# Optimization experiments

Hardware: AMD Instinct MI355X
Metric: run time of the kernel (lower is better)

## Reference

```python
import jax, jax.numpy as jnp
import numpy as np

N_HEADS = 16
HEAD_DIM = 128
ROPE_DIM = 64
ROPE_BASE = 10000.0


def _rope(x, base):
    # x: (B, H, S, dim) -- standard rotate-half RoPE, positions = arange(S)
    B, H, S, dim = x.shape
    inv_freq = 1.0 / (base ** (jnp.arange(0, dim, 2, dtype=jnp.float32) / dim))
    pos = jnp.arange(S, dtype=jnp.float32)
    freqs = pos[:, None] * inv_freq[None, :]                  # (S, dim/2)
    emb = jnp.concatenate([freqs, freqs], axis=-1)            # (S, dim)
    cos = jnp.cos(emb).astype(x.dtype)[None, None]
    sin = jnp.sin(emb).astype(x.dtype)[None, None]
    x1, x2 = x[..., : dim // 2], x[..., dim // 2 :]
    rot = jnp.concatenate([-x2, x1], axis=-1)
    return x * cos + rot * sin


def setup_inputs() -> dict:
    key = jax.random.key(0)
    ks = jax.random.split(key, 7)
    B, S, D = 2, 2048, 2048
    s = 0.02
    return {
        "x": jax.random.normal(ks[0], (B, S, D), jnp.float32),
        "Wq": jax.random.normal(ks[1], (D, N_HEADS * HEAD_DIM), jnp.float32) * s,
        "Wq_rope": jax.random.normal(ks[2], (D, N_HEADS * ROPE_DIM), jnp.float32) * s,
        "Wkv_down": jax.random.normal(ks[3], (D, 512), jnp.float32) * s,
        "Wkv_up": jax.random.normal(ks[4], (512, 2 * N_HEADS * HEAD_DIM), jnp.float32) * s,
        "Wk_rope": jax.random.normal(ks[5], (D, ROPE_DIM), jnp.float32) * s,
        "Wo": jax.random.normal(ks[6], (D, D), jnp.float32) * s,
    }


def reference(x, Wq, Wq_rope, Wkv_down, Wkv_up, Wk_rope, Wo):
    B, S, D = x.shape
    H, hd, rd = N_HEADS, HEAD_DIM, ROPE_DIM

    # content and decoupled-RoPE queries
    q_c = (x @ Wq).reshape(B, S, H, hd).transpose(0, 2, 1, 3)        # (B,H,S,hd)
    q_r = (x @ Wq_rope).reshape(B, S, H, rd).transpose(0, 2, 1, 3)   # (B,H,S,rd)
    q_r = _rope(q_r, ROPE_BASE)

    # low-rank KV latent + shared rope key
    c_kv = x @ Wkv_down                                              # (B,S,r)
    k_r = _rope((x @ Wk_rope)[:, None, :, :], ROPE_BASE)             # (B,1,S,rd)

    kv = c_kv @ Wkv_up                                               # (B,S,2*H*hd)
    k_c, v = jnp.split(kv, 2, axis=-1)
    k_c = k_c.reshape(B, S, H, hd).transpose(0, 2, 1, 3)             # (B,H,S,hd)
    v = v.reshape(B, S, H, hd).transpose(0, 2, 1, 3)                 # (B,H,S,hd)

    q_full = jnp.concatenate([q_c, q_r], axis=-1)                    # (B,H,S,hd+rd)
    k_full = jnp.concatenate([k_c, jnp.broadcast_to(k_r, (B, H, S, rd))], axis=-1)

    scale = 1.0 / np.sqrt(hd + rd).astype(np.float32)
    scores = jnp.einsum("bhqd,bhkd->bhqk", q_full, k_full) * scale   # (B,H,S,S)
    mask = jnp.tril(jnp.ones((S, S), dtype=bool))
    scores = jnp.where(mask[None, None], scores, jnp.finfo(scores.dtype).min)
    attn = jax.nn.softmax(scores, axis=-1)

    out = jnp.einsum("bhqk,bhkd->bhqd", attn, v)                     # (B,H,S,hd)
    out = out.transpose(0, 2, 1, 3).reshape(B, S, D)
    return out @ Wo
```

## Files before the change

### kernel.cpp

```cpp
#include <hip/hip_runtime.h>
#include <hip/hip_bf16.h>
#include <cstdint>
#include <cstddef>

typedef unsigned short u16;
typedef __attribute__((ext_vector_type(8))) short short8;
typedef __attribute__((ext_vector_type(4))) float f32x4;
typedef __attribute__((ext_vector_type(16))) float f32x16;

__device__ __forceinline__ u16 f2bf(float f) {
    union { float f; uint32_t u; } v; v.f = f;
    uint32_t u = v.u;
    return (u16)((u + 0x7fffu + ((u >> 16) & 1u)) >> 16);
}
__device__ __forceinline__ float bf2f(u16 u) {
    union { uint32_t u; float f; } v; v.u = ((uint32_t)u) << 16;
    return v.f;
}
__device__ __forceinline__ float exp2_hw(float x) {
    float r;
    asm("v_exp_f32 %0, %1" : "=v"(r) : "v"(x));
    return r;
}
__device__ __forceinline__ uint32_t cvtpk(float lo, float hi) {
    uint32_t r;
    asm("v_cvt_pk_bf16_f32 %0, %1, %2" : "=v"(r) : "v"(lo), "v"(hi));
    return r;
}
__device__ __forceinline__ void permswap(uint32_t& a, uint32_t& b) {
    asm("v_permlane32_swap_b32 %0, %1" : "+v"(a), "+v"(b));
}
__device__ __forceinline__ float xhalf_max(float x) {
    union { float f; uint32_t u; } a, b; a.f = x; b.f = x;
    permswap(a.u, b.u);
    return fmaxf(a.f, b.f);
}
__device__ __forceinline__ float xhalf_sum(float x) {
    union { float f; uint32_t u; } a, b; a.f = x; b.f = x;
    permswap(a.u, b.u);
    return a.f + b.f;
}

__device__ __forceinline__ void async_cp16(const u16* g, u16* l) {
    __builtin_amdgcn_global_load_lds(
        (const __attribute__((address_space(1))) unsigned int*)g,
        (__attribute__((address_space(3))) unsigned int*)l, 16, 0, 0);
}

__global__ __launch_bounds__(256) void cast_f32_bf16(const float* __restrict__ in,
                                                     u16* __restrict__ out, int n) {
    int i = (blockIdx.x * 256 + threadIdx.x) * 4;
    if (i >= n) return;
    float4 v = *(const float4*)(in + i);
    ushort4 r;
    r.x = f2bf(v.x); r.y = f2bf(v.y); r.z = f2bf(v.z); r.w = f2bf(v.w);
    *(ushort4*)(out + i) = r;
}

__global__ __launch_bounds__(256) void transpose_cast(const float* __restrict__ W,
                                                      u16* __restrict__ Wt, int K, int N,
                                                      float smul) {
    __shared__ u16 tile[64][72];
    int kt = blockIdx.x * 64, nt = blockIdx.y * 64;
    int t = threadIdx.x;
#pragma unroll
    for (int i = 0; i < 16; i++) {
        int idx = t + i * 256; int kl = idx >> 6, nl = idx & 63;
        tile[kl][nl] = f2bf(W[(size_t)(kt + kl) * N + nt + nl] * smul);
    }
    __syncthreads();
#pragma unroll
    for (int i = 0; i < 16; i++) {
        int idx = t + i * 256; int nl = idx >> 6, kl = idx & 63;
        Wt[(size_t)(nt + nl) * K + kt + kl] = tile[kl][nl];
    }
}

template <int OUTF32, int KDIM, int NDIM>
__global__ __launch_bounds__(256) void gemm_bt(const u16* __restrict__ A, int lda,
                                               const u16* __restrict__ Bt,
                                               void* __restrict__ Cout, int ldc) {
    __shared__ __align__(16) u16 Al[128 * 32];
    __shared__ __align__(16) u16 Bl[128 * 32];
    int m0 = blockIdx.x * 128, n0 = blockIdx.y * 128;
    int t = threadIdx.x;
    int w = t >> 6, l = t & 63;
    int lm = l & 15, lq = l >> 4;
    int wm = (w >> 1) * 64, wn = (w & 1) * 64;
    f32x4 acc[4][4] = {};

    for (int k0 = 0; k0 < KDIM; k0 += 32) {
#pragma unroll
        for (int c = 0; c < 2; c++) {
            int chunk = w * 128 + c * 64 + l;
            int row = chunk >> 2, col8 = (chunk & 3) * 8;
            async_cp16(A + (size_t)(m0 + row) * lda + k0 + col8,
                       Al + (w * 128 + c * 64) * 8);
            int brow = n0 + row;
            if (NDIM % 128 != 0) { if (brow >= NDIM) brow = NDIM - 1; }
            async_cp16(Bt + (size_t)brow * KDIM + k0 + col8,
                       Bl + (w * 128 + c * 64) * 8);
        }
        __syncthreads();
        short8 af[4], bfr[4];
#pragma unroll
        for (int mt = 0; mt < 4; mt++)
            af[mt] = *(const short8*)(Al + (wm + mt * 16 + lm) * 32 + lq * 8);
#pragma unroll
        for (int nt = 0; nt < 4; nt++)
            bfr[nt] = *(const short8*)(Bl + (wn + nt * 16 + lm) * 32 + lq * 8);
#pragma unroll
        for (int mt = 0; mt < 4; mt++)
#pragma unroll
            for (int nt = 0; nt < 4; nt++)
                acc[mt][nt] = __builtin_amdgcn_mfma_f32_16x16x32_bf16(af[mt], bfr[nt], acc[mt][nt], 0, 0, 0);
        __syncthreads();
    }
#pragma unroll
    for (int mt = 0; mt < 4; mt++) {
#pragma unroll
        for (int nt = 0; nt < 4; nt++) {
            int col = n0 + wn + nt * 16 + lm;
            if (col < NDIM) {
#pragma unroll
                for (int r = 0; r < 4; r++) {
                    int row = m0 + wm + mt * 16 + lq * 4 + r;
                    if (OUTF32) ((float*)Cout)[(size_t)row * ldc + col] = acc[mt][nt][r];
                    else        ((u16*)Cout)[(size_t)row * ldc + col] = f2bf(acc[mt][nt][r]);
                }
            }
        }
    }
}

template <int KDIM>
__global__ __launch_bounds__(256, 2) void gemm_rg(const u16* __restrict__ A, int lda,
                                                  const u16* __restrict__ Bt,
                                                  u16* __restrict__ C, int ldc) {
    __shared__ __align__(16) u16 Ab[3][128 * 32];
    __shared__ __align__(16) u16 Bb[3][256 * 32];
    const int nk = KDIM / 32;
    int m0 = blockIdx.x * 128, n0 = blockIdx.y * 256;
    int t = threadIdx.x, w = t >> 6, l = t & 63;
    int lm = l & 15, lq = l >> 4;
    int wn = w * 64;

    const u16* Apt[2]; const u16* Bpt[4];
    int ad[2], bd[4];
#pragma unroll
    for (int g = 0; g < 2; g++) {
        int c = t + g * 256, row = c >> 2;
        int col = ((c & 3) ^ ((row >> 1) & 3)) * 8;
        Apt[g] = A + (size_t)(m0 + row) * lda + col;
        ad[g] = (w * 64 + g * 256) * 8;
    }
#pragma unroll
    for (int g = 0; g < 4; g++) {
        int c = t + g * 256, row = c >> 2;
        int col = ((c & 3) ^ ((row >> 1) & 3)) * 8;
        Bpt[g] = Bt + (size_t)(n0 + row) * KDIM + col;
        bd[g] = (w * 64 + g * 256) * 8;
    }
    auto stage = [&](int ks, int buf) {
        int ko = ks * 32;
#pragma unroll
        for (int g = 0; g < 2; g++) async_cp16(Apt[g] + ko, Ab[buf] + ad[g]);
#pragma unroll
        for (int g = 0; g < 4; g++) async_cp16(Bpt[g] + ko, Bb[buf] + bd[g]);
    };

    int slot = (lq ^ ((lm >> 1) & 3)) * 8;

    f32x4 acc[8][4] = {};
    stage(0, 0); stage(1, 1);
    asm volatile("s_waitcnt vmcnt(6)" ::: "memory");
    __builtin_amdgcn_s_barrier();

    int bc = 0;
    for (int ks = 0; ks < nk; ks++) {
        int bs = (bc + 2 >= 3) ? bc - 1 : bc + 2;
        if (ks + 2 < nk) stage(ks + 2, bs);
        const u16* Al = Ab[bc];
        const u16* Bl = Bb[bc];
        short8 bfr[4], af[8];
#pragma unroll
        for (int nt = 0; nt < 4; nt++)
            bfr[nt] = *(const short8*)(Bl + (wn + nt * 16 + lm) * 32 + slot);
#pragma unroll
        for (int mt = 0; mt < 8; mt++)
            af[mt] = *(const short8*)(Al + (mt * 16 + lm) * 32 + slot);
        __builtin_amdgcn_s_setprio(1);
#pragma unroll
        for (int mt = 0; mt < 8; mt++)
#pragma unroll
            for (int nt = 0; nt < 4; nt++)
                acc[mt][nt] = __builtin_amdgcn_mfma_f32_16x16x32_bf16(af[mt], bfr[nt], acc[mt][nt], 0, 0, 0);
        __builtin_amdgcn_s_setprio(0);
        if (ks + 2 < nk)      { asm volatile("s_waitcnt vmcnt(6)" ::: "memory"); }
        else if (ks + 1 < nk) { asm volatile("s_waitcnt vmcnt(0)" ::: "memory"); }
        if (ks + 1 < nk) __builtin_amdgcn_s_barrier();
        bc = (bc + 1 == 3) ? 0 : bc + 1;
    }

#pragma unroll
    for (int mt = 0; mt < 8; mt++)
#pragma unroll
        for (int nt = 0; nt < 4; nt++) {
            int col = n0 + wn + nt * 16 + lm;
            u16* cp = C + (size_t)(m0 + mt * 16 + lq * 4) * ldc + col;
#pragma unroll
            for (int r = 0; r < 4; r++)
                cp[(size_t)r * ldc] = f2bf(acc[mt][nt][r]);
        }
}

__global__ __launch_bounds__(256) void rope_kernel(u16* __restrict__ x, int rows,
                                                   int nheads, int Smask, int stride) {
    int i = blockIdx.x * 256 + threadIdx.x;
    int total = rows * nheads * 32;
    if (i >= total) return;
    int j = i & 31;
    int h = (i >> 5) % nheads;
    int row = i / (32 * nheads);
    int pos = row & Smask;
    float f = exp2f((float)j * -0.4152410118609828f);
    float ang = (float)pos * f;
    float c = cosf(ang), s = sinf(ang);
    u16* p = x + (size_t)row * stride + h * 64 + j;
    float x1 = bf2f(p[0]), x2 = bf2f(p[32]);
    p[0]  = f2bf(x1 * c - x2 * s);
    p[32] = f2bf(x2 * c + x1 * s);
}

__global__ __launch_bounds__(256) void transpose_v(const u16* __restrict__ kv,
                                                   u16* __restrict__ vt, int S) {
    __shared__ u16 tile[64][72];
    int bh = blockIdx.z; int b = bh >> 4, h = bh & 15;
    int s0 = blockIdx.x * 64, d0 = blockIdx.y * 64;
    int t = threadIdx.x;
#pragma unroll
    for (int i = 0; i < 16; i++) {
        int idx = t + i * 256; int sl = idx >> 6, dl = idx & 63;
        tile[sl][dl] = kv[(size_t)(b * S + s0 + sl) * 4096 + 2048 + h * 128 + d0 + dl];
    }
    __syncthreads();
#pragma unroll
    for (int i = 0; i < 16; i++) {
        int idx = t + i * 256; int dl = idx >> 6, sl = idx & 63;
        vt[((size_t)(bh * 128 + d0 + dl)) * S + s0 + sl] = tile[sl][dl];
    }
}

__global__ __launch_bounds__(256, 2) void mla_attn(const u16* __restrict__ qc, int qcs,
                                                   const u16* __restrict__ qr, int qrs,
                                                   const u16* __restrict__ kvbuf,
                                                   const u16* __restrict__ kr, int krs,
                                                   const u16* __restrict__ vt,
                                                   u16* __restrict__ out, int S) {
    __shared__ __align__(16) u16 Kl[64 * 200];
    __shared__ __align__(16) u16 Vl[128 * 72];
    const float NEG = -1e30f;
    int bh = blockIdx.x; int b = bh >> 4, h = bh & 15;
    int y = blockIdx.y;
    int qt = (y < 8) ? (15 - y) : (y - 8);
    int t = threadIdx.x, w = t >> 6, l = t & 63;
    int ln = l & 31, hi = l >> 5;

    short8 kreg[6], vreg[4];
    auto load_tile = [&](int kbase) {
#pragma unroll
        for (int c = 0; c < 6; c++) {
            int idx = t + c * 256;
            int row = idx / 24, col = (idx % 24) * 8;
            const u16* src = (col < 128)
                ? kvbuf + (size_t)(b * S + kbase + row) * 4096 + h * 128 + col
                : kr + (size_t)(b * S + kbase + row) * krs + (col - 128);
            kreg[c] = *(const short8*)src;
        }
#pragma unroll
        for (int c = 0; c < 4; c++) {
            int idx = t + c * 256;
            int row = idx >> 3, col = (idx & 7) * 8;
            vreg[c] = *(const short8*)(vt + ((size_t)bh * 128 + row) * S + kbase + col);
        }
    };

    int qrow = qt * 128 + w * 32;
    int ntiles = 2 * qt + 2;

    short8 bq[12];
    {
        const u16* qc_row = qc + (size_t)(b * S + qrow + ln) * qcs + h * 128;
#pragma unroll
        for (int ks = 0; ks < 8; ks++) bq[ks] = *(const short8*)(qc_row + ks * 16 + hi * 8);
        const u16* qr_row = qr + (size_t)(b * S + qrow + ln) * qrs + h * 64;
#pragma unroll
        for (int ks = 0; ks < 4; ks++) bq[8 + ks] = *(const short8*)(qr_row + ks * 16 + hi * 8);
    }

    f32x16 o[4] = {};
    float m_s = 0.0f, l_s = 0.f;

    load_tile(0);
    for (int kt = 0; kt < ntiles; kt++) {
        int kbase = kt * 64;
        __syncthreads();
#pragma unroll
        for (int c = 0; c < 6; c++) {
            int idx = t + c * 256;
            int row = idx / 24, col = (idx % 24) * 8;
            *(short8*)(Kl + row * 200 + col) = kreg[c];
        }
#pragma unroll
        for (int c = 0; c < 4; c++) {
            int idx = t + c * 256;
            int row = idx >> 3, col = (idx & 7) * 8;
            *(short8*)(Vl + row * 72 + col) = vreg[c];
        }
        __syncthreads();
        if (kt + 1 < ntiles) load_tile(kbase + 64);

        if (kbase > qrow + 31) continue;

        f32x16 sacc[2] = {};
        __builtin_amdgcn_s_setprio(1);
#pragma unroll
        for (int ks = 0; ks < 12; ks++) {
            short8 ak0 = *(const short8*)(Kl + ln * 200 + ks * 16 + hi * 8);
            short8 ak1 = *(const short8*)(Kl + (32 + ln) * 200 + ks * 16 + hi * 8);
            sacc[0] = __builtin_amdgcn_mfma_f32_32x32x16_bf16(ak0, bq[ks], sacc[0], 0, 0, 0);
            sacc[1] = __builtin_amdgcn_mfma_f32_32x32x16_bf16(ak1, bq[ks], sacc[1], 0, 0, 0);
        }
        __builtin_amdgcn_s_setprio(0);

        if (kbase + 63 > qrow) {
            int qi = qrow + ln;
#pragma unroll
            for (int kt2 = 0; kt2 < 2; kt2++)
#pragma unroll
                for (int r = 0; r < 16; r++) {
                    int key = kbase + kt2 * 32 + (r & 3) + 8 * (r >> 2) + 4 * hi;
                    if (key > qi) sacc[kt2][r] = NEG;
                }
        }

        float m01 = NEG, m23 = NEG;
#pragma unroll
        for (int r = 0; r < 16; r += 2) {
            m01 = fmaxf(m01, fmaxf(sacc[0][r], sacc[0][r + 1]));
            m23 = fmaxf(m23, fmaxf(sacc[1][r], sacc[1][r + 1]));
        }
        float mx = xhalf_max(fmaxf(m01, m23));
        if (!__all(mx - m_s <= 8.0f)) {
            float mnew = fmaxf(m_s, mx);
            float alpha = exp2_hw(m_s - mnew);
            m_s = mnew;
            l_s *= alpha;
#pragma unroll
            for (int dt = 0; dt < 4; dt++) o[dt] *= alpha;
        }

        float rs = 0.f;
        short8 bp[2][2];
#pragma unroll
        for (int kt2 = 0; kt2 < 2; kt2++) {
            float p[16];
#pragma unroll
            for (int r = 0; r < 16; r++) p[r] = exp2_hw(sacc[kt2][r] - m_s);
#pragma unroll
            for (int r = 0; r < 16; r += 4)
                rs += (p[r] + p[r + 1]) + (p[r + 2] + p[r + 3]);
            uint32_t c0 = cvtpk(p[0], p[1]),  c1 = cvtpk(p[2], p[3]);
            uint32_t c2 = cvtpk(p[4], p[5]),  c3 = cvtpk(p[6], p[7]);
            permswap(c0, c2); permswap(c1, c3);
            union { uint32_t u[4]; short8 s; } f0 = {{c0, c1, c2, c3}};
            bp[kt2][0] = f0.s;
            uint32_t c4 = cvtpk(p[8], p[9]),   c5 = cvtpk(p[10], p[11]);
            uint32_t c6 = cvtpk(p[12], p[13]), c7 = cvtpk(p[14], p[15]);
            permswap(c4, c6); permswap(c5, c7);
            union { uint32_t u[4]; short8 s; } f1 = {{c4, c5, c6, c7}};
            bp[kt2][1] = f1.s;
        }
        l_s += xhalf_sum(rs);

        __builtin_amdgcn_s_setprio(1);
#pragma unroll
        for (int kt2 = 0; kt2 < 2; kt2++)
#pragma unroll
            for (int s = 0; s < 2; s++)
#pragma unroll
                for (int dt = 0; dt < 4; dt++) {
                    short8 av = *(const short8*)(Vl + (dt * 32 + ln) * 72 + kt2 * 32 + s * 16 + hi * 8);
                    o[dt] = __builtin_amdgcn_mfma_f32_32x32x16_bf16(av, bp[kt2][s], o[dt], 0, 0, 0);
                }
        __builtin_amdgcn_s_setprio(0);
    }

    float inv = 1.0f / l_s;
    u16* orow = out + (size_t)(b * S + qrow + ln) * 2048 + h * 128;
#pragma unroll
    for (int dt = 0; dt < 4; dt++)
#pragma unroll
        for (int g = 0; g < 4; g++) {
            ushort4 pk4;
            pk4.x = f2bf(o[dt][g * 4 + 0] * inv);
            pk4.y = f2bf(o[dt][g * 4 + 1] * inv);
            pk4.z = f2bf(o[dt][g * 4 + 2] * inv);
            pk4.w = f2bf(o[dt][g * 4 + 3] * inv);
            *(ushort4*)(orow + dt * 32 + g * 8 + hi * 4) = pk4;
        }
}

extern "C" void kernel_launch(void* const* d_in, const int* in_sizes, int n_in,
                              void* d_out, int out_size, void* d_ws, size_t ws_size,
                              hipStream_t stream) {
    const int B = 2, S = 2048, D = 2048, H = 16;
    const int M = B * S;
    const int NPpad = 3840;
    const float scale = 0.07216878364870323f * 1.4426950408889634f;
    const float* x    = (const float*)d_in[0];
    const float* Wq   = (const float*)d_in[1];
    const float* Wqr  = (const float*)d_in[2];
    const float* Wkvd = (const float*)d_in[3];
    const float* Wkvu = (const float*)d_in[4];
    const float* Wkr  = (const float*)d_in[5];
    const float* Wo   = (const float*)d_in[6];

    u16* p = (u16*)d_ws;
    u16* xb     = p; p += (size_t)M * D;
    u16* WprojT = p; p += (size_t)NPpad * 2048;
    u16* WkvuT  = p; p += (size_t)4096 * 512;
    u16* WoT    = p; p += (size_t)2048 * 2048;
    u16* proj   = p; p += (size_t)M * NPpad;
    u16* kv     = p; p += (size_t)M * 4096;
    u16* v_t    = p; p += (size_t)B * H * 128 * S;
    u16* attn   = p; p += (size_t)M * 2048;

    u16* q_c = proj;
    u16* q_r = proj + 2048;
    u16* ckv = proj + 3072;
    u16* k_r = proj + 3584;

    cast_f32_bf16<<<(M * D) / 4 / 256, 256, 0, stream>>>(x, xb, M * D);
    transpose_cast<<<dim3(32, 32), 256, 0, stream>>>(Wq,   WprojT,               2048, 2048, scale);
    transpose_cast<<<dim3(32, 16), 256, 0, stream>>>(Wqr,  WprojT + 2048 * 2048, 2048, 1024, scale);
    transpose_cast<<<dim3(32, 8),  256, 0, stream>>>(Wkvd, WprojT + 3072 * 2048, 2048, 512, 1.0f);
    transpose_cast<<<dim3(32, 1),  256, 0, stream>>>(Wkr,  WprojT + 3584 * 2048, 2048, 64, 1.0f);
    transpose_cast<<<dim3(8, 64),  256, 0, stream>>>(Wkvu, WkvuT, 512, 4096, 1.0f);
    transpose_cast<<<dim3(32, 32), 256, 0, stream>>>(Wo,   WoT,   2048, 2048, 1.0f);

    gemm_rg<2048><<<dim3(32, 15), 256, 0, stream>>>(xb, 2048, WprojT, proj, NPpad);

    rope_kernel<<<(M * 16 * 32) / 256, 256, 0, stream>>>(q_r, M, 16, S - 1, NPpad);
    rope_kernel<<<(M * 32) / 256, 256, 0, stream>>>(k_r, M, 1, S - 1, NPpad);

    gemm_rg<512><<<dim3(32, 16), 256, 0, stream>>>(ckv, NPpad, WkvuT, kv, 4096);
    transpose_v<<<dim3(32, 2, 32), 256, 0, stream>>>(kv, v_t, S);

    mla_attn<<<dim3(32, 16), 256, 0, stream>>>(q_c, NPpad, q_r, NPpad, kv, k_r, NPpad,
                                               v_t, attn, S);

    gemm_bt<1, 2048, 2048><<<dim3(32, 16), 256, 0, stream>>>(attn, 2048, WoT, d_out, 2048);
}
```

Measured before the change: 375.1 us.

## Switch projection GEMM to 32x32 MFMA and merge weight-prep and RoPE launches

The register-blocked GEMM moves from 16x16x32 bf16 MFMA tiles to 32x32x16 tiles, changing the fragment loads, LDS swizzle indexing and epilogue layout. The aim is fewer LDS reads per MFMA and better matrix-core throughput. Six weight transpose-cast launches are merged into one kernel that dispatches on block index, and the two RoPE launches become one, cutting launch overhead. The cost is more indexing logic, plus the risk of fragment-layout mistakes in the new MFMA shape.

```diff
diff --git a/kernel.cpp b/kernel.cpp
--- a/kernel.cpp
+++ b/kernel.cpp
@@ -57,11 +57,22 @@
     *(ushort4*)(out + i) = r;
 }
 
-__global__ __launch_bounds__(256) void transpose_cast(const float* __restrict__ W,
-                                                      u16* __restrict__ Wt, int K, int N,
-                                                      float smul) {
+__global__ __launch_bounds__(256) void transpose_cast_all(
+    const float* __restrict__ Wq, const float* __restrict__ Wqr,
+    const float* __restrict__ Wkvd, const float* __restrict__ Wkr,
+    const float* __restrict__ Wkvu, const float* __restrict__ Wo,
+    u16* __restrict__ WprojT, u16* __restrict__ WkvuT, u16* __restrict__ WoT,
+    float scale) {
+    int id = blockIdx.x;
+    const float* W; u16* Wt; int K, N, ktiles, tid; float smul;
+    if (id < 1024)      { W = Wq;   Wt = WprojT;              K = 2048; N = 2048; ktiles = 32; tid = id;        smul = scale; }
+    else if (id < 1536) { W = Wqr;  Wt = WprojT + 2048*2048;  K = 2048; N = 1024; ktiles = 32; tid = id - 1024; smul = scale; }
+    else if (id < 1792) { W = Wkvd; Wt = WprojT + 3072*2048;  K = 2048; N = 512;  ktiles = 32; tid = id - 1536; smul = 1.0f; }
+    else if (id < 1824) { W = Wkr;  Wt = WprojT + 3584*2048;  K = 2048; N = 64;   ktiles = 32; tid = id - 1792; smul = 1.0f; }
+    else if (id < 2336) { W = Wkvu; Wt = WkvuT;               K = 512;  N = 4096; ktiles = 8;  tid = id - 1824; smul = 1.0f; }
+    else                { W = Wo;   Wt = WoT;                 K = 2048; N = 2048; ktiles = 32; tid = id - 2336; smul = 1.0f; }
+    int kt = (tid % ktiles) * 64, nt = (tid / ktiles) * 64;
     __shared__ u16 tile[64][72];
-    int kt = blockIdx.x * 64, nt = blockIdx.y * 64;
     int t = threadIdx.x;
 #pragma unroll
     for (int i = 0; i < 16; i++) {
@@ -142,7 +153,7 @@
     const int nk = KDIM / 32;
     int m0 = blockIdx.x * 128, n0 = blockIdx.y * 256;
     int t = threadIdx.x, w = t >> 6, l = t & 63;
-    int lm = l & 15, lq = l >> 4;
+    int ln = l & 31, hi = l >> 5;
     int wn = w * 64;
 
     const u16* Apt[2]; const u16* Bpt[4];
@@ -169,9 +180,9 @@
         for (int g = 0; g < 4; g++) async_cp16(Bpt[g] + ko, Bb[buf] + bd[g]);
     };
 
-    int slot = (lq ^ ((lm >> 1) & 3)) * 8;
-
-    f32x4 acc[8][4] = {};
+    int sw = (ln >> 1) & 3;
+
+    f32x16 acc[4][2] = {};
     stage(0, 0); stage(1, 1);
     asm volatile("s_waitcnt vmcnt(6)" ::: "memory");
     __builtin_amdgcn_s_barrier();
@@ -182,19 +193,25 @@
         if (ks + 2 < nk) stage(ks + 2, bs);
         const u16* Al = Ab[bc];
         const u16* Bl = Bb[bc];
-        short8 bfr[4], af[8];
-#pragma unroll
-        for (int nt = 0; nt < 4; nt++)
-            bfr[nt] = *(const short8*)(Bl + (wn + nt * 16 + lm) * 32 + slot);
-#pragma unroll
-        for (int mt = 0; mt < 8; mt++)
-            af[mt] = *(const short8*)(Al + (mt * 16 + lm) * 32 + slot);
+        short8 af[4][2], bfr[2][2];
+#pragma unroll
+        for (int nt = 0; nt < 2; nt++)
+#pragma unroll
+            for (int kk = 0; kk < 2; kk++)
+                bfr[nt][kk] = *(const short8*)(Bl + (wn + nt * 32 + ln) * 32 + ((2 * kk + hi) ^ sw) * 8);
+#pragma unroll
+        for (int mt = 0; mt < 4; mt++)
+#pragma unroll
+            for (int kk = 0; kk < 2; kk++)
+                af[mt][kk] = *(const short8*)(Al + (mt * 32 + ln) * 32 + ((2 * kk + hi) ^ sw) * 8);
         __builtin_amdgcn_s_setprio(1);
 #pragma unroll
-        for (int mt = 0; mt < 8; mt++)
-#pragma unroll
-            for (int nt = 0; nt < 4; nt++)
-                acc[mt][nt] = __builtin_amdgcn_mfma_f32_16x16x32_bf16(af[mt], bfr[nt], acc[mt][nt], 0, 0, 0);
+        for (int kk = 0; kk < 2; kk++)
+#pragma unroll
+            for (int mt = 0; mt < 4; mt++)
+#pragma unroll
+                for (int nt = 0; nt < 2; nt++)
+                    acc[mt][nt] = __builtin_amdgcn_mfma_f32_32x32x16_bf16(af[mt][kk], bfr[nt][kk], acc[mt][nt], 0, 0, 0);
         __builtin_amdgcn_s_setprio(0);
         if (ks + 2 < nk)      { asm volatile("s_waitcnt vmcnt(6)" ::: "memory"); }
         else if (ks + 1 < nk) { asm volatile("s_waitcnt vmcnt(0)" ::: "memory"); }
@@ -203,30 +220,32 @@
     }
 
 #pragma unroll
-    for (int mt = 0; mt < 8; mt++)
-#pragma unroll
-        for (int nt = 0; nt < 4; nt++) {
-            int col = n0 + wn + nt * 16 + lm;
-            u16* cp = C + (size_t)(m0 + mt * 16 + lq * 4) * ldc + col;
-#pragma unroll
-            for (int r = 0; r < 4; r++)
-                cp[(size_t)r * ldc] = f2bf(acc[mt][nt][r]);
-        }
-}
-
-__global__ __launch_bounds__(256) void rope_kernel(u16* __restrict__ x, int rows,
-                                                   int nheads, int Smask, int stride) {
+    for (int mt = 0; mt < 4; mt++)
+#pragma unroll
+        for (int nt = 0; nt < 2; nt++) {
+            int col = n0 + wn + nt * 32 + ln;
+            u16* cp = C + (size_t)(m0 + mt * 32 + 4 * hi) * ldc + col;
+#pragma unroll
+            for (int g = 0; g < 4; g++)
+#pragma unroll
+                for (int r = 0; r < 4; r++)
+                    cp[(size_t)(g * 8 + r) * ldc] = f2bf(acc[mt][nt][g * 4 + r]);
+        }
+}
+
+__global__ __launch_bounds__(256) void rope_all(u16* __restrict__ xq, int rows,
+                                                int Smask, int stride) {
     int i = blockIdx.x * 256 + threadIdx.x;
-    int total = rows * nheads * 32;
-    if (i >= total) return;
+    if (i >= rows * 17 * 32) return;
     int j = i & 31;
-    int h = (i >> 5) % nheads;
-    int row = i / (32 * nheads);
+    int h = (i >> 5) % 17;
+    int row = i / (32 * 17);
     int pos = row & Smask;
     float f = exp2f((float)j * -0.4152410118609828f);
     float ang = (float)pos * f;
     float c = cosf(ang), s = sinf(ang);
-    u16* p = x + (size_t)row * stride + h * 64 + j;
+    int coff = (h < 16) ? h * 64 : 1536;
+    u16* p = xq + (size_t)row * stride + coff + j;
     float x1 = bf2f(p[0]), x2 = bf2f(p[32]);
     p[0]  = f2bf(x1 * c - x2 * s);
     p[32] = f2bf(x2 * c + x1 * s);
@@ -442,17 +461,12 @@
     u16* k_r = proj + 3584;
 
     cast_f32_bf16<<<(M * D) / 4 / 256, 256, 0, stream>>>(x, xb, M * D);
-    transpose_cast<<<dim3(32, 32), 256, 0, stream>>>(Wq,   WprojT,               2048, 2048, scale);
-    transpose_cast<<<dim3(32, 16), 256, 0, stream>>>(Wqr,  WprojT + 2048 * 2048, 2048, 1024, scale);
-    transpose_cast<<<dim3(32, 8),  256, 0, stream>>>(Wkvd, WprojT + 3072 * 2048, 2048, 512, 1.0f);
-    transpose_cast<<<dim3(32, 1),  256, 0, stream>>>(Wkr,  WprojT + 3584 * 2048, 2048, 64, 1.0f);
-    transpose_cast<<<dim3(8, 64),  256, 0, stream>>>(Wkvu, WkvuT, 512, 4096, 1.0f);
-    transpose_cast<<<dim3(32, 32), 256, 0, stream>>>(Wo,   WoT,   2048, 2048, 1.0f);
+    transpose_cast_all<<<3360, 256, 0, stream>>>(Wq, Wqr, Wkvd, Wkr, Wkvu, Wo,
+                                                 WprojT, WkvuT, WoT, scale);
 
     gemm_rg<2048><<<dim3(32, 15), 256, 0, stream>>>(xb, 2048, WprojT, proj, NPpad);
 
-    rope_kernel<<<(M * 16 * 32) / 256, 256, 0, stream>>>(q_r, M, 16, S - 1, NPpad);
-    rope_kernel<<<(M * 32) / 256, 256, 0, stream>>>(k_r, M, 1, S - 1, NPpad);
+    rope_all<<<(M * 17 * 32) / 256, 256, 0, stream>>>(q_r, M, S - 1, NPpad);
 
     gemm_rg<512><<<dim3(32, 16), 256, 0, stream>>>(ckv, NPpad, WkvuT, kv, 4096);
     transpose_v<<<dim3(32, 2, 32), 256, 0, stream>>>(kv, v_t, S);
```

Result: no change. 373.6 us (-0.4%).
